# Performance work log

Hardware: AMD Instinct MI355X
Metric: run time of the kernel (lower is better)

## Reference

```python
import jax, jax.numpy as jnp
import numpy as np

NUM_SLOTS = 8
PATCHES_PER_SLOT = 8  # num_select // num_slots, capped by N
TEMPERATURE = 0.1
NEG_INF = -10000.0


def _l2norm(x, eps=1e-6):
    # matches F.normalize: x / max(||x||, eps)
    n = jnp.sqrt(jnp.sum(x * x, axis=-1, keepdims=True))
    return x / jnp.maximum(n, eps)


def setup_inputs() -> dict:
    key = jax.random.key(0)
    k1, k2 = jax.random.split(key)
    local_feats = jax.random.normal(k1, (64, 1024, 768), dtype=jnp.float32)
    slots = jax.random.normal(k2, (1, NUM_SLOTS, 768), dtype=jnp.float32)
    return {"local_feats": local_feats, "slots": slots}


def reference(local_feats, slots):
    B, N, D = local_feats.shape
    K = slots.shape[1]
    slots_b = jnp.broadcast_to(slots, (B, K, D))

    x = local_feats.astype(jnp.float32)
    x_norm = _l2norm(x)
    s_norm = _l2norm(slots_b.astype(jnp.float32))

    # (B, K, N) cosine logits
    attn_logits = jnp.einsum('bkd,bnd->bkn', s_norm, x_norm)

    pps = min(PATCHES_PER_SLOT, N)
    topk_val, _ = jax.lax.top_k(attn_logits, pps)
    threshold = topk_val[:, :, -1:]  # (B, K, 1)

    mask_hard = (attn_logits >= threshold).astype(jnp.float32)
    mask_soft = jax.nn.sigmoid(attn_logits / TEMPERATURE)
    # straight-through estimator
    mask = jax.lax.stop_gradient(mask_hard - mask_soft) + mask_soft

    masked_logits = attn_logits * mask + NEG_INF * (1.0 - mask)
    attn = jax.nn.softmax(masked_logits, axis=-1)

    # img-space mask: max over slots -> (B, N, 1)
    img_space_mask = jnp.max(mask, axis=1)[..., None]

    # orthogonality loss on attention gram matrix
    gram = jnp.einsum('bkn,bjn->bkj', attn, attn)
    I = jnp.eye(K, dtype=jnp.float32)
    ortho_loss = jnp.mean(jnp.abs(gram - I[None, :, :]))

    # module returns the (unupdated) expanded slots, the ortho loss, and the mask
    return slots_b, ortho_loss, img_space_mask
```

## Files before the change

kernel.cpp:

```cpp
#include <hip/hip_runtime.h>
#include <math.h>

#define BB 64
#define NN 1024
#define DD 768
#define KK 8

#define WS_SNORM   0
#define WS_LOGITS  6144
#define WS_PART    (6144 + 524288)


template <int CTRL>
__device__ __forceinline__ float dpp_add(float x) {
    const int xi = __float_as_int(x);
    const int yi = __builtin_amdgcn_update_dpp(0, xi, CTRL, 0xF, 0xF, true);
    return x + __int_as_float(yi);
}

__global__ void k_broadcast(const float* __restrict__ slots, float* __restrict__ out) {
    const int b   = blockIdx.x / 6;
    const int r   = blockIdx.x % 6;
    const int idx = r * 256 + threadIdx.x;
    reinterpret_cast<float4*>(out)[b * 1536 + idx] =
        reinterpret_cast<const float4*>(slots)[idx];
}

__global__ void k_snorm(const float* __restrict__ slots, float* __restrict__ snorm) {
    const int k = blockIdx.x;
    const int t = threadIdx.x;
    const int lane = t & 63, wave = t >> 6;
    __shared__ float wsum[4];
    float s = 0.f;
    for (int j = t; j < DD; j += 256) {
        float v = slots[k * DD + j];
        s += v * v;
    }
#pragma unroll
    for (int off = 1; off < 64; off <<= 1) s += __shfl_xor(s, off, 64);
    if (lane == 0) wsum[wave] = s;
    __syncthreads();
    const float tot = wsum[0] + wsum[1] + wsum[2] + wsum[3];
    const float rn = 1.0f / fmaxf(sqrtf(tot), 1e-6f);
    for (int j = t; j < DD; j += 256) snorm[k * DD + j] = slots[k * DD + j] * rn;
}

__launch_bounds__(256)
__global__ void k_logits(const float* __restrict__ x, const float* __restrict__ snorm,
                         float* __restrict__ logits) {
    const int b     = blockIdx.x >> 4;
    const int chunk = blockIdx.x & 15;
    const int wave  = threadIdx.x >> 6;
    const int lane  = threadIdx.x & 63;
    const int b2 = (lane >> 2) & 1, b4 = (lane >> 4) & 1, b5 = (lane >> 5) & 1;

    float4 sreg[KK][3];
#pragma unroll
    for (int k = 0; k < KK; ++k)
#pragma unroll
        for (int j = 0; j < 3; ++j)
            sreg[k][j] = *reinterpret_cast<const float4*>(snorm + k * DD + j * 256 + lane * 4);

    const int n_base = chunk * 64 + wave * 16;

    auto compute_one = [&](int n, float4 c0, float4 c1, float4 c2) {
        float acc[KK];
#pragma unroll
        for (int q = 0; q < KK; ++q) acc[q] = 0.f;

#pragma unroll
        for (int k = 0; k < KK; ++k) {
            acc[k] = fmaf(c0.x, sreg[k][0].x, acc[k]);
            acc[k] = fmaf(c0.y, sreg[k][0].y, acc[k]);
            acc[k] = fmaf(c0.z, sreg[k][0].z, acc[k]);
            acc[k] = fmaf(c0.w, sreg[k][0].w, acc[k]);
            acc[k] = fmaf(c1.x, sreg[k][1].x, acc[k]);
            acc[k] = fmaf(c1.y, sreg[k][1].y, acc[k]);
            acc[k] = fmaf(c1.z, sreg[k][1].z, acc[k]);
            acc[k] = fmaf(c1.w, sreg[k][1].w, acc[k]);
            acc[k] = fmaf(c2.x, sreg[k][2].x, acc[k]);
            acc[k] = fmaf(c2.y, sreg[k][2].y, acc[k]);
            acc[k] = fmaf(c2.z, sreg[k][2].z, acc[k]);
            acc[k] = fmaf(c2.w, sreg[k][2].w, acc[k]);
        }
        float u = 0.f;
        u = fmaf(c0.x, c0.x, u); u = fmaf(c0.y, c0.y, u);
        u = fmaf(c0.z, c0.z, u); u = fmaf(c0.w, c0.w, u);
        u = fmaf(c1.x, c1.x, u); u = fmaf(c1.y, c1.y, u);
        u = fmaf(c1.z, c1.z, u); u = fmaf(c1.w, c1.w, u);
        u = fmaf(c2.x, c2.x, u); u = fmaf(c2.y, c2.y, u);
        u = fmaf(c2.z, c2.z, u); u = fmaf(c2.w, c2.w, u);

        float w[4];
#pragma unroll
        for (int j = 0; j < 4; ++j) {
            const float send = b2 ? acc[j] : acc[j + 4];
            const float keep = b2 ? acc[j + 4] : acc[j];
            w[j] = keep + __shfl_xor(send, 4, 64);
        }
        u += __shfl_xor(u, 4, 64);

        const float s0 = b4 ? w[0] : w[2];
        const float s1 = b4 ? w[1] : w[3];
        const float y0 = (b4 ? w[2] : w[0]) + __shfl_xor(s0, 16, 64);
        const float y1 = (b4 ? w[3] : w[1]) + __shfl_xor(s1, 16, 64);
        u += __shfl_xor(u, 16, 64);

        const float sz = b5 ? y0 : y1;
        float z = (b5 ? y1 : y0) + __shfl_xor(sz, 32, 64);
        u += __shfl_xor(u, 32, 64);

        z = dpp_add<0xB1>(z);   u = dpp_add<0xB1>(u);
        z = dpp_add<0x4E>(z);   u = dpp_add<0x4E>(u);
        z = dpp_add<0x128>(z);  u = dpp_add<0x128>(u);

        const float rn = 1.0f / fmaxf(sqrtf(u), 1e-6f);
        if ((lane & 11) == 0) {
            const int k = 4 * b2 + 2 * b4 + b5;
            logits[(((b << 3) + k) << 10) + n] = z * rn;
        }
    };

    const float4* xrow = reinterpret_cast<const float4*>(x + (long)(b * NN + n_base) * DD);
    float4 c0 = xrow[lane], c1 = xrow[64 + lane], c2 = xrow[128 + lane];

    for (int i = 0; i < 15; ++i) {
        const float4* xq = xrow + (i + 1) * (DD / 4);
        float4 p0 = xq[lane], p1 = xq[64 + lane], p2 = xq[128 + lane];
        compute_one(n_base + i, c0, c1, c2);
        c0 = p0; c1 = p1; c2 = p2;
    }
    compute_one(n_base + 15, c0, c1, c2);
}

__launch_bounds__(512)
__global__ void k_select(const float* __restrict__ logits, float* __restrict__ out_mask,
                         float* __restrict__ partials) {
    const int b = blockIdx.x;
    __shared__ float lds[KK][1032];
    __shared__ float thr[KK], rmax[KK], rsum[KK];
    __shared__ float gpart[8][64];
    const int t = threadIdx.x, lane = t & 63, wave = t >> 6;

    for (int f = t; f < KK * NN; f += 512) lds[f >> 10][f & 1023] = logits[b * (KK * NN) + f];
    __syncthreads();

    {
        const int k = wave;
        float v[16];
#pragma unroll
        for (int i = 0; i < 16; ++i) v[i] = lds[k][i * 64 + lane];
        float th = 0.f, mx = -1e30f;
        for (int e = 0; e < 8; ++e) {
            float lv = -1e30f; int li = 0;
#pragma unroll
            for (int i = 0; i < 16; ++i) {
                if (v[i] > lv) { lv = v[i]; li = i * 64 + lane; }
            }
#pragma unroll
            for (int off = 1; off < 64; off <<= 1) {
                const float ov = __shfl_xor(lv, off, 64);
                const int   oi = __shfl_xor(li, off, 64);
                if (ov > lv || (ov == lv && oi < li)) { lv = ov; li = oi; }
            }
            if (e == 0) mx = lv;
            th = lv;
#pragma unroll
            for (int i = 0; i < 16; ++i)
                if (i * 64 + lane == li) v[i] = -1e30f;
        }
        if (lane == 0) { thr[k] = th; rmax[k] = mx; }
    }
    __syncthreads();

    for (int n = t; n < NN; n += 512) {
        float m = 0.f;
#pragma unroll
        for (int k = 0; k < KK; ++k) m = fmaxf(m, (lds[k][n] >= thr[k]) ? 1.f : 0.f);
        out_mask[b * NN + n] = m;
    }
    __syncthreads();

    {
        const int k = wave;
        const float th = thr[k], mx = rmax[k];
        float s = 0.f;
#pragma unroll
        for (int i = 0; i < 16; ++i) {
            const int n = i * 64 + lane;
            const float lg = lds[k][n];
            const float p = (lg >= th) ? __expf(lg - mx) : 0.f;
            lds[k][n] = p;
            s += p;
        }
#pragma unroll
        for (int off = 1; off < 64; off <<= 1) s += __shfl_xor(s, off, 64);
        if (lane == 0) rsum[k] = s;
    }
    __syncthreads();

    {
        const int k = lane >> 3, j = lane & 7;
        float s = 0.f;
#pragma unroll 8
        for (int i = 0; i < 128; ++i) {
            const int n = (wave << 7) + i;
            s += lds[k][n] * lds[j][n];
        }
        gpart[wave][lane] = s;
    }
    __syncthreads();
    if (wave == 0) {
        const int k = lane >> 3, j = lane & 7;
        float g = 0.f;
#pragma unroll
        for (int w = 0; w < 8; ++w) g += gpart[w][lane];
        g *= (1.0f / rsum[k]) * (1.0f / rsum[j]);
        float d = fabsf(g - ((k == j) ? 1.f : 0.f));
#pragma unroll
        for (int off = 1; off < 64; off <<= 1) d += __shfl_xor(d, off, 64);
        if (lane == 0) partials[b] = d;
    }
}

__global__ void k_final(const float* __restrict__ partials, float* __restrict__ out_loss) {
    const int lane = threadIdx.x;
    float v = partials[lane];
#pragma unroll
    for (int off = 1; off < 64; off <<= 1) v += __shfl_xor(v, off, 64);
    if (lane == 0) out_loss[0] = v * (1.0f / 4096.0f);
}

extern "C" void kernel_launch(void* const* d_in, const int* in_sizes, int n_in,
                              void* d_out, int out_size, void* d_ws, size_t ws_size,
                              hipStream_t stream) {
    const float* x     = (const float*)d_in[0];
    const float* slots = (const float*)d_in[1];
    float* out = (float*)d_out;
    float* ws  = (float*)d_ws;

    float* snorm    = ws + WS_SNORM;
    float* logits   = ws + WS_LOGITS;
    float* partials = ws + WS_PART;

    float* out_slots = out;
    float* out_loss  = out + 393216;
    float* out_mask  = out + 393217;

    k_broadcast<<<dim3(384),     dim3(256), 0, stream>>>(slots, out_slots);
    k_snorm    <<<dim3(KK),      dim3(256), 0, stream>>>(slots, snorm);
    k_logits   <<<dim3(BB * 16), dim3(256), 0, stream>>>(x, snorm, logits);
    k_select   <<<dim3(BB),      dim3(512), 0, stream>>>(logits, out_mask, partials);
    k_final    <<<dim3(1),       dim3(64),  0, stream>>>(partials, out_loss);
}
```

Baseline: 297.9 us.

## Stage normalized slots in LDS and process two patch rows per iteration

The logits kernel no longer keeps all eight normalized slot vectors in registers (96 VGPRs of float4). Each block now copies them into shared memory, and the kernel processes two patch rows per step, reusing each LDS slot read across both rows. Loads for the next pair of rows are prefetched while the current pair is computed. The aim is lower register pressure, and so higher occupancy for this memory-bound streaming kernel, plus deeper memory parallelism. The cost is extra LDS traffic and a block-level barrier.

```diff
diff --git a/kernel.cpp b/kernel.cpp
--- a/kernel.cpp
+++ b/kernel.cpp
@@ -16,6 +16,51 @@
     const int xi = __float_as_int(x);
     const int yi = __builtin_amdgcn_update_dpp(0, xi, CTRL, 0xF, 0xF, true);
     return x + __int_as_float(yi);
+}
+
+__device__ __forceinline__ float dot12(const float4& a0, const float4& a1, const float4& a2,
+                                       const float4& b0, const float4& b1, const float4& b2) {
+    float r = 0.f;
+    r = fmaf(a0.x, b0.x, r); r = fmaf(a0.y, b0.y, r);
+    r = fmaf(a0.z, b0.z, r); r = fmaf(a0.w, b0.w, r);
+    r = fmaf(a1.x, b1.x, r); r = fmaf(a1.y, b1.y, r);
+    r = fmaf(a1.z, b1.z, r); r = fmaf(a1.w, b1.w, r);
+    r = fmaf(a2.x, b2.x, r); r = fmaf(a2.y, b2.y, r);
+    r = fmaf(a2.z, b2.z, r); r = fmaf(a2.w, b2.w, r);
+    return r;
+}
+
+__device__ __forceinline__ void reduce_store(float (&acc)[KK], float u, int n,
+                                             int lane, int b2, int b4, int b5,
+                                             int b, float* __restrict__ logits) {
+    float w[4];
+#pragma unroll
+    for (int j = 0; j < 4; ++j) {
+        const float send = b2 ? acc[j] : acc[j + 4];
+        const float keep = b2 ? acc[j + 4] : acc[j];
+        w[j] = keep + __shfl_xor(send, 4, 64);
+    }
+    u += __shfl_xor(u, 4, 64);
+
+    const float s0 = b4 ? w[0] : w[2];
+    const float s1 = b4 ? w[1] : w[3];
+    const float y0 = (b4 ? w[2] : w[0]) + __shfl_xor(s0, 16, 64);
+    const float y1 = (b4 ? w[3] : w[1]) + __shfl_xor(s1, 16, 64);
+    u += __shfl_xor(u, 16, 64);
+
+    const float sz = b5 ? y0 : y1;
+    float z = (b5 ? y1 : y0) + __shfl_xor(sz, 32, 64);
+    u += __shfl_xor(u, 32, 64);
+
+    z = dpp_add<0xB1>(z);   u = dpp_add<0xB1>(u);
+    z = dpp_add<0x4E>(z);   u = dpp_add<0x4E>(u);
+    z = dpp_add<0x128>(z);  u = dpp_add<0x128>(u);
+
+    const float rn = 1.0f / fmaxf(sqrtf(u), 1e-6f);
+    if ((lane & 11) == 0) {
+        const int k = 4 * b2 + 2 * b4 + b5;
+        logits[(((b << 3) + k) << 10) + n] = z * rn;
+    }
 }
 
 __global__ void k_broadcast(const float* __restrict__ slots, float* __restrict__ out) {
@@ -54,83 +99,42 @@
     const int lane  = threadIdx.x & 63;
     const int b2 = (lane >> 2) & 1, b4 = (lane >> 4) & 1, b5 = (lane >> 5) & 1;
 
-    float4 sreg[KK][3];
-#pragma unroll
-    for (int k = 0; k < KK; ++k)
-#pragma unroll
-        for (int j = 0; j < 3; ++j)
-            sreg[k][j] = *reinterpret_cast<const float4*>(snorm + k * DD + j * 256 + lane * 4);
+    __shared__ float4 sl[KK * 192];
+    for (int i = threadIdx.x; i < KK * 192; i += 256)
+        sl[i] = reinterpret_cast<const float4*>(snorm)[i];
+    __syncthreads();
 
     const int n_base = chunk * 64 + wave * 16;
-
-    auto compute_one = [&](int n, float4 c0, float4 c1, float4 c2) {
-        float acc[KK];
-#pragma unroll
-        for (int q = 0; q < KK; ++q) acc[q] = 0.f;
-
+    const float4* xrow = reinterpret_cast<const float4*>(x + (long)(b * NN + n_base) * DD);
+
+    auto compute_pair = [&](int n, const float4& a0, const float4& a1, const float4& a2,
+                                   const float4& e0, const float4& e1, const float4& e2) {
+        float accA[KK], accB[KK];
 #pragma unroll
         for (int k = 0; k < KK; ++k) {
-            acc[k] = fmaf(c0.x, sreg[k][0].x, acc[k]);
-            acc[k] = fmaf(c0.y, sreg[k][0].y, acc[k]);
-            acc[k] = fmaf(c0.z, sreg[k][0].z, acc[k]);
-            acc[k] = fmaf(c0.w, sreg[k][0].w, acc[k]);
-            acc[k] = fmaf(c1.x, sreg[k][1].x, acc[k]);
-            acc[k] = fmaf(c1.y, sreg[k][1].y, acc[k]);
-            acc[k] = fmaf(c1.z, sreg[k][1].z, acc[k]);
-            acc[k] = fmaf(c1.w, sreg[k][1].w, acc[k]);
-            acc[k] = fmaf(c2.x, sreg[k][2].x, acc[k]);
-            acc[k] = fmaf(c2.y, sreg[k][2].y, acc[k]);
-            acc[k] = fmaf(c2.z, sreg[k][2].z, acc[k]);
-            acc[k] = fmaf(c2.w, sreg[k][2].w, acc[k]);
-        }
-        float u = 0.f;
-        u = fmaf(c0.x, c0.x, u); u = fmaf(c0.y, c0.y, u);
-        u = fmaf(c0.z, c0.z, u); u = fmaf(c0.w, c0.w, u);
-        u = fmaf(c1.x, c1.x, u); u = fmaf(c1.y, c1.y, u);
-        u = fmaf(c1.z, c1.z, u); u = fmaf(c1.w, c1.w, u);
-        u = fmaf(c2.x, c2.x, u); u = fmaf(c2.y, c2.y, u);
-        u = fmaf(c2.z, c2.z, u); u = fmaf(c2.w, c2.w, u);
-
-        float w[4];
-#pragma unroll
-        for (int j = 0; j < 4; ++j) {
-            const float send = b2 ? acc[j] : acc[j + 4];
-            const float keep = b2 ? acc[j + 4] : acc[j];
-            w[j] = keep + __shfl_xor(send, 4, 64);
-        }
-        u += __shfl_xor(u, 4, 64);
-
-        const float s0 = b4 ? w[0] : w[2];
-        const float s1 = b4 ? w[1] : w[3];
-        const float y0 = (b4 ? w[2] : w[0]) + __shfl_xor(s0, 16, 64);
-        const float y1 = (b4 ? w[3] : w[1]) + __shfl_xor(s1, 16, 64);
-        u += __shfl_xor(u, 16, 64);
-
-        const float sz = b5 ? y0 : y1;
-        float z = (b5 ? y1 : y0) + __shfl_xor(sz, 32, 64);
-        u += __shfl_xor(u, 32, 64);
-
-        z = dpp_add<0xB1>(z);   u = dpp_add<0xB1>(u);
-        z = dpp_add<0x4E>(z);   u = dpp_add<0x4E>(u);
-        z = dpp_add<0x128>(z);  u = dpp_add<0x128>(u);
-
-        const float rn = 1.0f / fmaxf(sqrtf(u), 1e-6f);
-        if ((lane & 11) == 0) {
-            const int k = 4 * b2 + 2 * b4 + b5;
-            logits[(((b << 3) + k) << 10) + n] = z * rn;
-        }
+            const float4 s0 = sl[k * 192 + lane];
+            const float4 s1 = sl[k * 192 + 64 + lane];
+            const float4 s2 = sl[k * 192 + 128 + lane];
+            accA[k] = dot12(a0, a1, a2, s0, s1, s2);
+            accB[k] = dot12(e0, e1, e2, s0, s1, s2);
+        }
+        const float uA = dot12(a0, a1, a2, a0, a1, a2);
+        const float uB = dot12(e0, e1, e2, e0, e1, e2);
+        reduce_store(accA, uA, n,     lane, b2, b4, b5, b, logits);
+        reduce_store(accB, uB, n + 1, lane, b2, b4, b5, b, logits);
     };
 
-    const float4* xrow = reinterpret_cast<const float4*>(x + (long)(b * NN + n_base) * DD);
-    float4 c0 = xrow[lane], c1 = xrow[64 + lane], c2 = xrow[128 + lane];
-
-    for (int i = 0; i < 15; ++i) {
-        const float4* xq = xrow + (i + 1) * (DD / 4);
-        float4 p0 = xq[lane], p1 = xq[64 + lane], p2 = xq[128 + lane];
-        compute_one(n_base + i, c0, c1, c2);
-        c0 = p0; c1 = p1; c2 = p2;
-    }
-    compute_one(n_base + 15, c0, c1, c2);
+    float4 a0 = xrow[lane],        a1 = xrow[64 + lane],  a2 = xrow[128 + lane];
+    float4 e0 = xrow[192 + lane],  e1 = xrow[256 + lane], e2 = xrow[320 + lane];
+
+    for (int i = 0; i < 7; ++i) {
+        const float4* xq = xrow + (2 * i + 2) * 192;
+        float4 pA0 = xq[lane],        pA1 = xq[64 + lane],  pA2 = xq[128 + lane];
+        float4 pB0 = xq[192 + lane],  pB1 = xq[256 + lane], pB2 = xq[320 + lane];
+        compute_pair(n_base + 2 * i, a0, a1, a2, e0, e1, e2);
+        a0 = pA0; a1 = pA1; a2 = pA2; e0 = pB0; e1 = pB1; e2 = pB2;
+    }
+    compute_pair(n_base + 14, a0, a1, a2, e0, e1, e2);
 }
 
 __launch_bounds__(512)
```

Measured after the change: 299.8 us. No clear change (+0.6%).
